# Kernel tuning notes

Hardware: AMD Instinct MI355X
Metric: run time of the kernel (lower is better)

The kernel has to match this reference:

```python
import jax, jax.numpy as jnp
import numpy as np

B, C, H, W = 16, 2048, 14, 14
D = 8192  # output_dim


def setup_inputs() -> dict:
    key = jax.random.key(0)
    k1, k2, k3, k4, k5 = jax.random.split(key, 5)
    x = jax.random.normal(k1, (B, C, H, W), dtype=jnp.float32)
    h1 = jax.random.randint(k2, (C,), 0, D, dtype=jnp.int32)
    h2 = jax.random.randint(k3, (C,), 0, D, dtype=jnp.int32)
    s1 = jax.random.randint(k4, (C,), 0, 2, dtype=jnp.int32)
    s2 = jax.random.randint(k5, (C,), 0, 2, dtype=jnp.int32)
    return {"x": x, "h1": h1, "h2": h2, "s1": s1, "s2": s2}


def _count_sketch(x_flat, h, sign, out_dim):
    # x_flat: (B, C, HW); h: (C,) hash buckets; sign: (C,) in {-1,+1}
    xs = x_flat * sign[None, :, None]
    sketch = jnp.zeros((x_flat.shape[0], out_dim, x_flat.shape[2]), dtype=x_flat.dtype)
    return sketch.at[:, h, :].add(xs)  # scatter-add over channel -> bucket


def reference(x, h1, h2, s1, s2):
    b, c, hgt, wid = x.shape
    x_flat = x.reshape(b, c, hgt * wid).astype(jnp.float32)
    sg1 = (2 * s1 - 1).astype(jnp.float32)
    sg2 = (2 * s2 - 1).astype(jnp.float32)
    sketch1 = _count_sketch(x_flat, h1, sg1, D)  # (B, D, HW)
    sketch2 = _count_sketch(x_flat, h2, sg2, D)
    fft1 = jnp.fft.fft(sketch1, axis=1)
    fft2 = jnp.fft.fft(sketch2, axis=1)
    cbp = jnp.fft.ifft(fft1 * fft2, axis=1).real  # circular conv per location
    cbp = cbp.sum(axis=-1)  # sum-pool over HW -> (B, D)
    cbp = jnp.sign(cbp) * jnp.sqrt(jnp.abs(cbp) + 1e-5)  # signed sqrt
    norm = jnp.maximum(jnp.linalg.norm(cbp, axis=1, keepdims=True), 1e-12)
    cbp = cbp / norm  # L2 normalize (matches F.normalize eps=1e-12)
    return cbp.astype(x.dtype)
```

## Files before the change

kernel.cpp:

```cpp
#include <hip/hip_runtime.h>
#include <hip/hip_bf16.h>
#include <math.h>

#define FFT_N 8192
#define HWN 196
#define CCH 2048
#define BATCH 16
#define PBLK 14
#define PPER 14
#define NPAIR 7

#define ZPAD(i) ((i) + ((i) >> 4))
#define ZSZ 8704

__device__ __forceinline__ int kof(int j) {
    return ((j >> 11) & 3) | (((j >> 9) & 3) << 2) | (((j >> 7) & 3) << 4) |
           (((j >> 5) & 3) << 6) | (((j >> 3) & 3) << 8) | (((j >> 1) & 3) << 10) |
           ((j & 1) << 12);
}
__device__ __forceinline__ int pof(int k) {
    return ((k & 3) << 11) | (((k >> 2) & 3) << 9) | (((k >> 4) & 3) << 7) |
           (((k >> 6) & 3) << 5) | (((k >> 8) & 3) << 3) | (((k >> 10) & 3) << 1) |
           ((k >> 12) & 1);
}

#define TW_TOTAL 1706

__device__ __forceinline__ float2 cmul(float2 a, float2 b) {
    return make_float2(a.x * b.x - a.y * b.y, a.x * b.y + a.y * b.x);
}

__device__ __forceinline__ void bf4(float2* z, int i0, int i1, int i2, int i3,
                                    float2 w1, float2 w2, float2 w3) {
    float2 a = z[i0], b = z[i1], c = z[i2], d = z[i3];
    float t0r = a.x + c.x, t0i = a.y + c.y, t1r = a.x - c.x, t1i = a.y - c.y;
    float t2r = b.x + d.x, t2i = b.y + d.y, t3r = b.x - d.x, t3i = b.y - d.y;
    float2 u0 = make_float2(t0r + t2r, t0i + t2i);
    float2 u2 = make_float2(t0r - t2r, t0i - t2i);
    float2 u1 = make_float2(t1r + t3i, t1i - t3r);
    float2 u3 = make_float2(t1r - t3i, t1i + t3r);
    z[i0] = u0;
    z[i1] = cmul(u1, w1);
    z[i2] = cmul(u2, w2);
    z[i3] = cmul(u3, w3);
}

template <int Q4, int OFF, bool DUAL>
__device__ __forceinline__ void pass4(float2* z0, float2* z1, const float2* T, int tid) {
#pragma unroll
    for (int it = 0; it < 2; ++it) {
        int u = tid + 1024 * it;
        int o = u & (Q4 - 1);
        int base = ((u & ~(Q4 - 1)) << 2) | o;
        int i0 = ZPAD(base), i1 = ZPAD(base + Q4);
        int i2 = ZPAD(base + 2 * Q4), i3 = ZPAD(base + 3 * Q4);
        float2 w1;
        if constexpr (Q4 == 2048) {
            w1 = T[o & 1023];
            if (o & 1024) {
                const float r = 0.70710678118654752f;
                w1 = make_float2(r * (w1.x + w1.y), r * (w1.y - w1.x));
            }
        } else {
            w1 = T[OFF + o];
        }
        float2 w2 = make_float2(w1.x * w1.x - w1.y * w1.y, 2.f * w1.x * w1.y);
        float2 w3 = cmul(w1, w2);
        bf4(z0, i0, i1, i2, i3, w1, w2, w3);
        if constexpr (DUAL) bf4(z1, i0, i1, i2, i3, w1, w2, w3);
    }
    __syncthreads();
}

template <bool DUAL>
__device__ __forceinline__ void fft8192d(float2* z0, float2* z1, const float2* T, int tid) {
    pass4<2048, 0, DUAL>(z0, z1, T, tid);
    pass4<512, 1024, DUAL>(z0, z1, T, tid);
    pass4<128, 1536, DUAL>(z0, z1, T, tid);
    pass4<32, 1664, DUAL>(z0, z1, T, tid);
    pass4<8, 1696, DUAL>(z0, z1, T, tid);
    pass4<2, 1704, DUAL>(z0, z1, T, tid);
#pragma unroll
    for (int it = 0; it < 4; ++it) {
        int u = tid + 1024 * it;
        int i0 = ZPAD(2 * u), i1 = ZPAD(2 * u + 1);
        float2 a = z0[i0], b = z0[i1];
        z0[i0] = make_float2(a.x + b.x, a.y + b.y);
        z0[i1] = make_float2(a.x - b.x, a.y - b.y);
        if constexpr (DUAL) {
            float2 c = z1[i0], d = z1[i1];
            z1[i0] = make_float2(c.x + d.x, c.y + d.y);
            z1[i1] = make_float2(c.x - d.x, c.y - d.y);
        }
    }
    __syncthreads();
}

__device__ __forceinline__ void build_tables(float2* T, int tid) {
    const float w0 = -7.66990393942820573e-4f;
    {
        float s, c; sincosf(w0 * (float)tid, &s, &c); T[tid] = make_float2(c, s);
    }
    if (tid < 512) {
        float s, c; sincosf(w0 * (float)(tid * 4), &s, &c); T[1024 + tid] = make_float2(c, s);
    }
    if (tid < 128) {
        float s, c; sincosf(w0 * (float)(tid * 16), &s, &c); T[1536 + tid] = make_float2(c, s);
    }
    if (tid < 32) {
        float s, c; sincosf(w0 * (float)(tid * 64), &s, &c); T[1664 + tid] = make_float2(c, s);
    }
    if (tid < 8) {
        float s, c; sincosf(w0 * (float)(tid * 256), &s, &c); T[1696 + tid] = make_float2(c, s);
    }
    if (tid < 2) {
        float s, c; sincosf(w0 * (float)(tid * 1024), &s, &c); T[1704 + tid] = make_float2(c, s);
    }
}

__global__ __launch_bounds__(1024) void cbp_fwd(
    const float* __restrict__ x, const int* __restrict__ h1,
    const int* __restrict__ h2, const int* __restrict__ s1,
    const int* __restrict__ s2, float2* __restrict__ acc) {
    __shared__ float2 zs[2][ZSZ];
    __shared__ float2 T[TW_TOTAL];
    int tid = threadIdx.x;
    int b = blockIdx.x / PBLK;
    int pb = blockIdx.x % PBLK;

    int c0 = tid, c1 = tid + 1024;

    const float2* pA = (const float2*)(x + ((size_t)b * CCH + c0) * HWN + pb * PPER);
    const float2* pB = (const float2*)(x + ((size_t)b * CCH + c1) * HWN + pb * PPER);
    float2 xA[NPAIR], xB[NPAIR];
#pragma unroll
    for (int q = 0; q < NPAIR; ++q) xA[q] = pA[q];
#pragma unroll
    for (int q = 0; q < NPAIR; ++q) xB[q] = pB[q];

    build_tables(T, tid);

    int h1a = ZPAD(h1[c0]), h2a = ZPAD(h2[c0]);
    int h1b = ZPAD(h1[c1]), h2b = ZPAD(h2[c1]);
    float g1a = (float)(2 * s1[c0] - 1), g2a = (float)(2 * s2[c0] - 1);
    float g1b = (float)(2 * s1[c1] - 1), g2b = (float)(2 * s2[c1] - 1);

    float accR[8], accI[8];
#pragma unroll
    for (int s = 0; s < 8; s++) { accR[s] = 0.f; accI[s] = 0.f; }

    float2* z0 = zs[0];
    float2* z1 = zs[1];
    float2* zf2 = (float2*)zs;

#pragma unroll
    for (int ii = 0; ii < NPAIR; ++ii) {
        float2 va = xA[ii];
        float2 vb = xB[ii];

#pragma unroll
        for (int i = 0; i < 17; ++i) zf2[tid + 1024 * i] = make_float2(0.f, 0.f);
        __syncthreads();

        atomicAdd(&z0[h1a].x, g1a * va.x);
        atomicAdd(&z0[h2a].y, g2a * va.x);
        atomicAdd(&z0[h1b].x, g1b * vb.x);
        atomicAdd(&z0[h2b].y, g2b * vb.x);
        atomicAdd(&z1[h1a].x, g1a * va.y);
        atomicAdd(&z1[h2a].y, g2a * va.y);
        atomicAdd(&z1[h1b].x, g1b * vb.y);
        atomicAdd(&z1[h2b].y, g2b * vb.y);
        __syncthreads();

        fft8192d<true>(z0, z1, T, tid);

#pragma unroll
        for (int s = 0; s < 8; s++) {
            int j = tid + 1024 * s;
            int k = kof(j);
            int m = (FFT_N - k) & (FFT_N - 1);
            int j2 = pof(m);
            int pj = ZPAD(j), pj2 = ZPAD(j2);
            float2 a0 = z0[pj], b0 = z0[pj2];
            float2 a1 = z1[pj], b1 = z1[pj2];
            float Dr = (a0.x * a0.x - a0.y * a0.y) - (b0.x * b0.x - b0.y * b0.y)
                     + (a1.x * a1.x - a1.y * a1.y) - (b1.x * b1.x - b1.y * b1.y);
            float Di = 2.f * (a0.x * a0.y + b0.x * b0.y)
                     + 2.f * (a1.x * a1.y + b1.x * b1.y);
            accR[s] += 0.25f * Di;
            accI[s] -= 0.25f * Dr;
        }
        __syncthreads();
    }

    float2* ab = acc + (size_t)b * FFT_N;
#pragma unroll
    for (int s = 0; s < 8; s++) {
        int j = tid + 1024 * s;
        atomicAdd(&ab[j].x, accR[s]);
        atomicAdd(&ab[j].y, accI[s]);
    }
}

__global__ __launch_bounds__(1024) void cbp_inv(
    const float2* __restrict__ acc, float* __restrict__ out) {
    __shared__ float2 z[ZSZ];
    __shared__ float2 T[TW_TOTAL];
    __shared__ float red[20];
    int tid = threadIdx.x;
    int b = blockIdx.x;

    build_tables(T, tid);

    const float2* ab = acc + (size_t)b * FFT_N;
#pragma unroll
    for (int s = 0; s < 8; s++) {
        int j = tid + 1024 * s;
        float2 v = ab[j];
        z[ZPAD(kof(j))] = make_float2(v.x, -v.y);
    }
    __syncthreads();

    fft8192d<false>(z, z, T, tid);

    float sv[8];
    float ss = 0.f;
#pragma unroll
    for (int s = 0; s < 8; s++) {
        int j = tid + 1024 * s;
        float v = z[ZPAD(j)].x * (1.f / (float)FFT_N);
        float r = copysignf(sqrtf(fabsf(v) + 1e-5f), v);
        sv[s] = r;
        ss += r * r;
    }
#pragma unroll
    for (int m = 32; m >= 1; m >>= 1) ss += __shfl_xor(ss, m);
    int wave = tid >> 6, lane = tid & 63;
    if (lane == 0) red[wave] = ss;
    __syncthreads();
    if (tid == 0) {
        float tot = 0.f;
        for (int w = 0; w < 16; w++) tot += red[w];
        red[16] = fmaxf(sqrtf(tot), 1e-12f);
    }
    __syncthreads();
    float inv = 1.f / red[16];
    float* ob = out + (size_t)b * FFT_N;
#pragma unroll
    for (int s = 0; s < 8; s++) {
        int j = tid + 1024 * s;
        ob[kof(j)] = sv[s] * inv;
    }
}

extern "C" void kernel_launch(void* const* d_in, const int* in_sizes, int n_in,
                              void* d_out, int out_size, void* d_ws, size_t ws_size,
                              hipStream_t stream) {
    const float* x = (const float*)d_in[0];
    const int* h1 = (const int*)d_in[1];
    const int* h2 = (const int*)d_in[2];
    const int* s1 = (const int*)d_in[3];
    const int* s2 = (const int*)d_in[4];
    float* out = (float*)d_out;
    float2* acc = (float2*)d_ws;

    hipMemsetAsync(acc, 0, (size_t)BATCH * FFT_N * sizeof(float2), stream);
    cbp_fwd<<<BATCH * PBLK, 1024, 0, stream>>>(x, h1, h2, s1, s2, acc);
    cbp_inv<<<BATCH, 1024, 0, stream>>>(acc, (float*)out);
}
```

Baseline: 330.1 us.

## Replace radix-4 FFT passes with radix-8 passes to cut LDS round trips

The 8192-point shared-memory FFT now uses four radix-8 passes plus a final radix-2 pass, replacing six radix-4 passes plus radix-2. The digit-reversal maps and twiddle tables are updated to match. This removes two LDS read/write sweeps and two barriers per FFT, and it does fewer twiddle multiplies overall. In exchange each thread holds more live registers, and the launch bounds now ask for a minimum occupancy of 4 on both kernels, which could cause spilling.

```diff
diff --git a/kernel.cpp b/kernel.cpp
--- a/kernel.cpp
+++ b/kernel.cpp
@@ -13,84 +13,91 @@
 #define ZPAD(i) ((i) + ((i) >> 4))
 #define ZSZ 8704
 
-__device__ __forceinline__ int kof(int j) {
-    return ((j >> 11) & 3) | (((j >> 9) & 3) << 2) | (((j >> 7) & 3) << 4) |
-           (((j >> 5) & 3) << 6) | (((j >> 3) & 3) << 8) | (((j >> 1) & 3) << 10) |
-           ((j & 1) << 12);
-}
-__device__ __forceinline__ int pof(int k) {
-    return ((k & 3) << 11) | (((k >> 2) & 3) << 9) | (((k >> 4) & 3) << 7) |
-           (((k >> 6) & 3) << 5) | (((k >> 8) & 3) << 3) | (((k >> 10) & 3) << 1) |
-           ((k >> 12) & 1);
-}
-
-#define TW_TOTAL 1706
+__device__ __forceinline__ int kof8(int j) {
+    return ((j >> 10) & 7) | (((j >> 7) & 7) << 3) | (((j >> 4) & 7) << 6) |
+           (((j >> 1) & 7) << 9) | ((j & 1) << 12);
+}
+__device__ __forceinline__ int pof8(int k) {
+    return ((k & 7) << 10) | (((k >> 3) & 7) << 7) | (((k >> 6) & 7) << 4) |
+           (((k >> 9) & 7) << 1) | ((k >> 12) & 1);
+}
+
+#define TW_TOTAL 1170
 
 __device__ __forceinline__ float2 cmul(float2 a, float2 b) {
     return make_float2(a.x * b.x - a.y * b.y, a.x * b.y + a.y * b.x);
 }
-
-__device__ __forceinline__ void bf4(float2* z, int i0, int i1, int i2, int i3,
-                                    float2 w1, float2 w2, float2 w3) {
-    float2 a = z[i0], b = z[i1], c = z[i2], d = z[i3];
-    float t0r = a.x + c.x, t0i = a.y + c.y, t1r = a.x - c.x, t1i = a.y - c.y;
-    float t2r = b.x + d.x, t2i = b.y + d.y, t3r = b.x - d.x, t3i = b.y - d.y;
-    float2 u0 = make_float2(t0r + t2r, t0i + t2i);
-    float2 u2 = make_float2(t0r - t2r, t0i - t2i);
-    float2 u1 = make_float2(t1r + t3i, t1i - t3r);
-    float2 u3 = make_float2(t1r - t3i, t1i + t3r);
-    z[i0] = u0;
-    z[i1] = cmul(u1, w1);
-    z[i2] = cmul(u2, w2);
-    z[i3] = cmul(u3, w3);
-}
-
-template <int Q4, int OFF, bool DUAL>
-__device__ __forceinline__ void pass4(float2* z0, float2* z1, const float2* T, int tid) {
-#pragma unroll
-    for (int it = 0; it < 2; ++it) {
-        int u = tid + 1024 * it;
-        int o = u & (Q4 - 1);
-        int base = ((u & ~(Q4 - 1)) << 2) | o;
-        int i0 = ZPAD(base), i1 = ZPAD(base + Q4);
-        int i2 = ZPAD(base + 2 * Q4), i3 = ZPAD(base + 3 * Q4);
-        float2 w1;
-        if constexpr (Q4 == 2048) {
-            w1 = T[o & 1023];
-            if (o & 1024) {
-                const float r = 0.70710678118654752f;
-                w1 = make_float2(r * (w1.x + w1.y), r * (w1.y - w1.x));
-            }
-        } else {
-            w1 = T[OFF + o];
-        }
-        float2 w2 = make_float2(w1.x * w1.x - w1.y * w1.y, 2.f * w1.x * w1.y);
-        float2 w3 = cmul(w1, w2);
-        bf4(z0, i0, i1, i2, i3, w1, w2, w3);
-        if constexpr (DUAL) bf4(z1, i0, i1, i2, i3, w1, w2, w3);
-    }
+__device__ __forceinline__ float2 cadd(float2 a, float2 b) { return make_float2(a.x + b.x, a.y + b.y); }
+__device__ __forceinline__ float2 csub(float2 a, float2 b) { return make_float2(a.x - b.x, a.y - b.y); }
+
+__device__ __forceinline__ void bf8(float2* z, int i0, int i1, int i2, int i3,
+                                    int i4, int i5, int i6, int i7,
+                                    float2 w1, float2 w2, float2 w3, float2 w4,
+                                    float2 w5, float2 w6, float2 w7) {
+    float2 a0 = z[i0], a1 = z[i1], a2 = z[i2], a3 = z[i3];
+    float2 a4 = z[i4], a5 = z[i5], a6 = z[i6], a7 = z[i7];
+    float2 b0 = cadd(a0, a4), b1 = cadd(a1, a5), b2 = cadd(a2, a6), b3 = cadd(a3, a7);
+    float2 c0 = csub(a0, a4), c1 = csub(a1, a5), c2 = csub(a2, a6), c3 = csub(a3, a7);
+    const float r = 0.70710678118654752f;
+    c1 = make_float2(r * (c1.x + c1.y), r * (c1.y - c1.x));
+    c2 = make_float2(c2.y, -c2.x);
+    c3 = make_float2(r * (c3.y - c3.x), -r * (c3.x + c3.y));
+    float2 t0, t1, t2, t3;
+    t0 = cadd(b0, b2); t1 = csub(b0, b2); t2 = cadd(b1, b3); t3 = csub(b1, b3);
+    float2 E0 = cadd(t0, t2);
+    float2 E1 = make_float2(t1.x + t3.y, t1.y - t3.x);
+    float2 E2 = csub(t0, t2);
+    float2 E3 = make_float2(t1.x - t3.y, t1.y + t3.x);
+    t0 = cadd(c0, c2); t1 = csub(c0, c2); t2 = cadd(c1, c3); t3 = csub(c1, c3);
+    float2 O0 = cadd(t0, t2);
+    float2 O1 = make_float2(t1.x + t3.y, t1.y - t3.x);
+    float2 O2 = csub(t0, t2);
+    float2 O3 = make_float2(t1.x - t3.y, t1.y + t3.x);
+    z[i0] = E0;
+    z[i1] = cmul(O0, w1);
+    z[i2] = cmul(E1, w2);
+    z[i3] = cmul(O1, w3);
+    z[i4] = cmul(E2, w4);
+    z[i5] = cmul(O2, w5);
+    z[i6] = cmul(E3, w6);
+    z[i7] = cmul(O3, w7);
+}
+
+template <int Q, int TOFF, bool DUAL>
+__device__ __forceinline__ void pass8(float2* z0, float2* z1, const float2* T, int tid) {
+    int o = tid & (Q - 1);
+    int base = ((tid & ~(Q - 1)) << 3) | o;
+    int i0 = ZPAD(base), i1 = ZPAD(base + Q), i2 = ZPAD(base + 2 * Q), i3 = ZPAD(base + 3 * Q);
+    int i4 = ZPAD(base + 4 * Q), i5 = ZPAD(base + 5 * Q), i6 = ZPAD(base + 6 * Q), i7 = ZPAD(base + 7 * Q);
+    float2 w1 = T[TOFF + o];
+    float2 w2 = cmul(w1, w1);
+    float2 w3 = cmul(w2, w1);
+    float2 w4 = cmul(w2, w2);
+    float2 w5 = cmul(w2, w3);
+    float2 w6 = cmul(w3, w3);
+    float2 w7 = cmul(w3, w4);
+    bf8(z0, i0, i1, i2, i3, i4, i5, i6, i7, w1, w2, w3, w4, w5, w6, w7);
+    if constexpr (DUAL) bf8(z1, i0, i1, i2, i3, i4, i5, i6, i7, w1, w2, w3, w4, w5, w6, w7);
     __syncthreads();
 }
 
 template <bool DUAL>
 __device__ __forceinline__ void fft8192d(float2* z0, float2* z1, const float2* T, int tid) {
-    pass4<2048, 0, DUAL>(z0, z1, T, tid);
-    pass4<512, 1024, DUAL>(z0, z1, T, tid);
-    pass4<128, 1536, DUAL>(z0, z1, T, tid);
-    pass4<32, 1664, DUAL>(z0, z1, T, tid);
-    pass4<8, 1696, DUAL>(z0, z1, T, tid);
-    pass4<2, 1704, DUAL>(z0, z1, T, tid);
+    pass8<1024, 0, DUAL>(z0, z1, T, tid);
+    pass8<128, 1024, DUAL>(z0, z1, T, tid);
+    pass8<16, 1152, DUAL>(z0, z1, T, tid);
+    pass8<2, 1168, DUAL>(z0, z1, T, tid);
 #pragma unroll
     for (int it = 0; it < 4; ++it) {
         int u = tid + 1024 * it;
         int i0 = ZPAD(2 * u), i1 = ZPAD(2 * u + 1);
         float2 a = z0[i0], b = z0[i1];
-        z0[i0] = make_float2(a.x + b.x, a.y + b.y);
-        z0[i1] = make_float2(a.x - b.x, a.y - b.y);
+        z0[i0] = cadd(a, b);
+        z0[i1] = csub(a, b);
         if constexpr (DUAL) {
             float2 c = z1[i0], d = z1[i1];
-            z1[i0] = make_float2(c.x + d.x, c.y + d.y);
-            z1[i1] = make_float2(c.x - d.x, c.y - d.y);
+            z1[i0] = cadd(c, d);
+            z1[i1] = csub(c, d);
         }
     }
     __syncthreads();
@@ -101,24 +108,18 @@
     {
         float s, c; sincosf(w0 * (float)tid, &s, &c); T[tid] = make_float2(c, s);
     }
-    if (tid < 512) {
-        float s, c; sincosf(w0 * (float)(tid * 4), &s, &c); T[1024 + tid] = make_float2(c, s);
-    }
     if (tid < 128) {
-        float s, c; sincosf(w0 * (float)(tid * 16), &s, &c); T[1536 + tid] = make_float2(c, s);
-    }
-    if (tid < 32) {
-        float s, c; sincosf(w0 * (float)(tid * 64), &s, &c); T[1664 + tid] = make_float2(c, s);
-    }
-    if (tid < 8) {
-        float s, c; sincosf(w0 * (float)(tid * 256), &s, &c); T[1696 + tid] = make_float2(c, s);
+        float s, c; sincosf(w0 * (float)(tid * 8), &s, &c); T[1024 + tid] = make_float2(c, s);
+    }
+    if (tid < 16) {
+        float s, c; sincosf(w0 * (float)(tid * 64), &s, &c); T[1152 + tid] = make_float2(c, s);
     }
     if (tid < 2) {
-        float s, c; sincosf(w0 * (float)(tid * 1024), &s, &c); T[1704 + tid] = make_float2(c, s);
-    }
-}
-
-__global__ __launch_bounds__(1024) void cbp_fwd(
+        float s, c; sincosf(w0 * (float)(tid * 512), &s, &c); T[1168 + tid] = make_float2(c, s);
+    }
+}
+
+__global__ __launch_bounds__(1024, 4) void cbp_fwd(
     const float* __restrict__ x, const int* __restrict__ h1,
     const int* __restrict__ h2, const int* __restrict__ s1,
     const int* __restrict__ s2, float2* __restrict__ acc) {
@@ -177,9 +178,9 @@
 #pragma unroll
         for (int s = 0; s < 8; s++) {
             int j = tid + 1024 * s;
-            int k = kof(j);
+            int k = kof8(j);
             int m = (FFT_N - k) & (FFT_N - 1);
-            int j2 = pof(m);
+            int j2 = pof8(m);
             int pj = ZPAD(j), pj2 = ZPAD(j2);
             float2 a0 = z0[pj], b0 = z0[pj2];
             float2 a1 = z1[pj], b1 = z1[pj2];
@@ -202,7 +203,7 @@
     }
 }
 
-__global__ __launch_bounds__(1024) void cbp_inv(
+__global__ __launch_bounds__(1024, 4) void cbp_inv(
     const float2* __restrict__ acc, float* __restrict__ out) {
     __shared__ float2 z[ZSZ];
     __shared__ float2 T[TW_TOTAL];
@@ -217,7 +218,7 @@
     for (int s = 0; s < 8; s++) {
         int j = tid + 1024 * s;
         float2 v = ab[j];
-        z[ZPAD(kof(j))] = make_float2(v.x, -v.y);
+        z[ZPAD(kof8(j))] = make_float2(v.x, -v.y);
     }
     __syncthreads();
 
@@ -249,7 +250,7 @@
 #pragma unroll
     for (int s = 0; s < 8; s++) {
         int j = tid + 1024 * s;
-        ob[kof(j)] = sv[s] * inv;
+        ob[kof8(j)] = sv[s] * inv;
     }
 }
 
```

After: 283.4 us. 1.16x faster.
